# Optimization experiments

Measured on AMD Instinct MI355X. Metric: run time of the kernel, lower is better.

Reference implementation:

```python
import jax, jax.numpy as jnp
import numpy as np

B, N, H = 32, 1024, 256
ALPHA = 0.2  # leaky relu slope
NEG_INF = -1e12


def setup_inputs() -> dict:
    key = jax.random.key(0)
    k1, k2, k3, k4, k5, k6 = jax.random.split(key, 6)
    inp = jax.random.normal(k1, (B, N, H), dtype=jnp.float32)
    A = (jax.random.uniform(k2, (B, N, N)) < 0.05).astype(jnp.float32)
    l = jnp.sort(jax.random.randint(k3, (B, 2), 0, N), axis=1)
    # xavier-uniform(gain=1.414) approximated; exact init values are irrelevant for correctness
    lim_w = 1.414 * np.sqrt(6.0 / (H + H))
    W_i = jax.random.uniform(k4, (H, H), minval=-lim_w, maxval=lim_w, dtype=jnp.float32)
    W_c = jax.random.uniform(k5, (H, H), minval=-lim_w, maxval=lim_w, dtype=jnp.float32)
    lim_a = 1.414 * np.sqrt(6.0 / (2 * H + 1))
    a = jax.random.uniform(k6, (2 * H, 1), minval=-lim_a, maxval=lim_a, dtype=jnp.float32)
    return {"inp": inp, "A": A, "l": l, "W_i": W_i, "W_c": W_c, "a": a}


def reference(inp, A, l, W_i, W_c, a):
    # eval mode: dropout is identity (training=False)
    n = inp.shape[1]
    h = inp.shape[2]
    Wh_i = jnp.einsum('bnh,he->bne', inp, W_i)
    Wh_c = jnp.einsum('bnh,he->bne', inp, W_c)
    # vectorized replacement of the per-batch Wh[index][i:j] = Wh_i[index][i:j] loop
    idx = jnp.arange(n)
    sel = (idx[None, :] >= l[:, 0:1]) & (idx[None, :] < l[:, 1:2])  # [B,N]
    Wh = jnp.where(sel[:, :, None], Wh_i, Wh_c)
    # additive attention scores
    Wh1 = Wh @ a[:h, :]  # [B,N,1]
    Wh2 = Wh @ a[h:, :]  # [B,N,1]
    A_ = A + jnp.eye(n, dtype=A.dtype)
    e = jax.nn.leaky_relu((Wh1 + jnp.swapaxes(Wh2, 1, 2)) * A_, ALPHA)
    att = jnp.where(A_ > 0, e, NEG_INF)
    att = jax.nn.softmax(att, axis=2)
    h_prime = jnp.einsum('bnm,bme->bne', att, Wh)
    return jax.nn.elu(h_prime)  # concat=True
```

## Files before the change

kernel.cpp:

```cpp
#include <hip/hip_runtime.h>
#include <hip/hip_bf16.h>
#include <stdint.h>

#define B_ 32
#define N_ 1024
#define H_ 256

typedef short bf16x8 __attribute__((ext_vector_type(8)));
typedef float floatx4 __attribute__((ext_vector_type(4)));

__device__ inline unsigned short f2bs(float x) {
    __hip_bfloat16 h = __float2bfloat16(x);
    return __builtin_bit_cast(unsigned short, h);
}

__global__ __launch_bounds__(256)
void k_uvec(const float* __restrict__ Wi, const float* __restrict__ Wc,
            const float* __restrict__ a, float* __restrict__ U) {
    int k = blockIdx.x;
    int t = threadIdx.x;
    float wi = Wi[k * H_ + t];
    float wc = Wc[k * H_ + t];
    float a1 = a[t], a2 = a[H_ + t];
    float p0 = wi * a1, p1 = wc * a1, p2 = wi * a2, p3 = wc * a2;
    for (int off = 32; off; off >>= 1) {
        p0 += __shfl_xor(p0, off);
        p1 += __shfl_xor(p1, off);
        p2 += __shfl_xor(p2, off);
        p3 += __shfl_xor(p3, off);
    }
    __shared__ float red[4][4];
    int w = t >> 6;
    if ((t & 63) == 0) { red[w][0] = p0; red[w][1] = p1; red[w][2] = p2; red[w][3] = p3; }
    __syncthreads();
    if (t == 0) {
        U[0 * H_ + k] = red[0][0] + red[1][0] + red[2][0] + red[3][0];
        U[1 * H_ + k] = red[0][1] + red[1][1] + red[2][1] + red[3][1];
        U[2 * H_ + k] = red[0][2] + red[1][2] + red[2][2] + red[3][2];
        U[3 * H_ + k] = red[0][3] + red[1][3] + red[2][3] + red[3][3];
    }
}

__global__ __launch_bounds__(256)
void k_prep(const float* __restrict__ Wi, const float* __restrict__ Wc,
            unsigned short* __restrict__ WtFi, unsigned short* __restrict__ WtFc) {
    __shared__ float tile[64][65];
    int mat = blockIdx.x >> 4;
    int tr = ((blockIdx.x >> 2) & 3) * 64;
    int tc = (blockIdx.x & 3) * 64;
    const float* W = mat ? Wc : Wi;
    unsigned short* WtF = mat ? WtFc : WtFi;
    int t = threadIdx.x;
    int rr = t >> 2, c4 = (t & 3) * 16;
    const float* src = W + (size_t)(tr + rr) * H_ + tc + c4;
#pragma unroll
    for (int j = 0; j < 4; ++j) {
        float4 v = *reinterpret_cast<const float4*>(src + j * 4);
        tile[rr][c4 + 4 * j + 0] = v.x;
        tile[rr][c4 + 4 * j + 1] = v.y;
        tile[rr][c4 + 4 * j + 2] = v.z;
        tile[rr][c4 + 4 * j + 3] = v.w;
    }
    __syncthreads();
#pragma unroll
    for (int h = 0; h < 2; ++h) {
        int s = h * 256 + t;
        int ksl = s >> 8;
        int cl  = (s >> 6) & 3;
        int ll  = s & 63;
        int m16v = ll & 15, quadv = ll >> 4;
        int nloc = cl * 16 + m16v;
        int kb = ksl * 32 + quadv * 8;
        unsigned int pk[4];
#pragma unroll
        for (int jj = 0; jj < 4; ++jj) {
            unsigned short lo = f2bs(tile[kb + 2 * jj][nloc]);
            unsigned short hi = f2bs(tile[kb + 2 * jj + 1][nloc]);
            pk[jj] = (unsigned int)lo | ((unsigned int)hi << 16);
        }
        int ksg = (tr >> 5) + ksl;
        int cg  = (tc >> 4) + cl;
        *reinterpret_cast<uint4*>(WtF + ((size_t)(ksg * 16 + cg) * 64 + ll) * 8) =
            *reinterpret_cast<uint4*>(pk);
    }
}

__global__ __launch_bounds__(256)
void k_gemm(const float* __restrict__ inp, const int* __restrict__ l,
            const unsigned short* __restrict__ WtFi, const unsigned short* __restrict__ WtFc,
            unsigned short* __restrict__ WhF, const float* __restrict__ U,
            float* __restrict__ Wh1, float* __restrict__ Wh2) {
    __shared__ unsigned short bbuf[2][4096];
    int blk = blockIdx.x;
    int b  = blk >> 5;
    int r0 = ((blk >> 1) & 15) * 64;
    int n0 = (blk & 1) * 128;
    int t = threadIdx.x;
    int w = t >> 6;
    int lane = t & 63;
    int quad = lane >> 4, m16 = lane & 15;
    int rowb = r0 + w * 16;

    int l0 = l[2 * b], l1 = l[2 * b + 1];
    bool allI = (l0 <= r0) && (r0 + 64 <= l1);
    bool allC = (l1 <= r0) || (l0 >= r0 + 64);
    int npass = (allI || allC) ? 1 : 2;

    int row = rowb + m16;
    bool sel = (row >= l0) && (row < l1);
    const float* xrow = inp + ((size_t)(b * N_ + row)) * H_;
    const float* u1 = U + (sel ? 0 : H_);
    const float* u2 = U + 2 * H_ + (sel ? 0 : H_);
    bool doWh = (n0 == 0);
    float d1 = 0.f, d2 = 0.f;

    unsigned short* fb = WhF + (size_t)b * (N_ * H_);
    int cb = n0 >> 4;

    int j0 = rowb + quad * 4;
    int ksO = j0 >> 5;
    int laneF = m16 + 16 * ((j0 & 31) >> 3);
    int jj0 = j0 & 7;

    for (int pass = 0; pass < npass; ++pass) {
        const unsigned short* WtF =
            (npass == 1) ? (allI ? WtFi : WtFc) : (pass == 0 ? WtFi : WtFc);
        const unsigned short* gbase = WtF + cb * 512;

        floatx4 acc[8];
#pragma unroll
        for (int c = 0; c < 8; ++c) acc[c] = (floatx4){0.f, 0.f, 0.f, 0.f};

        {
            uint4 v0 = *reinterpret_cast<const uint4*>(gbase + (size_t)t * 8);
            uint4 v1 = *reinterpret_cast<const uint4*>(gbase + (size_t)(256 + t) * 8);
            *reinterpret_cast<uint4*>(&bbuf[0][t * 8]) = v0;
            *reinterpret_cast<uint4*>(&bbuf[0][(256 + t) * 8]) = v1;
        }
        for (int ks = 0; ks < 8; ++ks) {
            __syncthreads();
            uint4 v0, v1;
            if (ks < 7) {
                v0 = *reinterpret_cast<const uint4*>(gbase + (size_t)(ks + 1) * 8192 + t * 8);
                v1 = *reinterpret_cast<const uint4*>(gbase + (size_t)(ks + 1) * 8192 + (256 + t) * 8);
            }
            const float4 xa = *reinterpret_cast<const float4*>(xrow + ks * 32 + quad * 8);
            const float4 xb = *reinterpret_cast<const float4*>(xrow + ks * 32 + quad * 8 + 4);
            if (pass == 0 && doWh) {
                const float4 ua = *reinterpret_cast<const float4*>(u1 + ks * 32 + quad * 8);
                const float4 ub = *reinterpret_cast<const float4*>(u1 + ks * 32 + quad * 8 + 4);
                const float4 va = *reinterpret_cast<const float4*>(u2 + ks * 32 + quad * 8);
                const float4 vb = *reinterpret_cast<const float4*>(u2 + ks * 32 + quad * 8 + 4);
                d1 += xa.x * ua.x + xa.y * ua.y + xa.z * ua.z + xa.w * ua.w
                    + xb.x * ub.x + xb.y * ub.y + xb.z * ub.z + xb.w * ub.w;
                d2 += xa.x * va.x + xa.y * va.y + xa.z * va.z + xa.w * va.w
                    + xb.x * vb.x + xb.y * vb.y + xb.z * vb.z + xb.w * vb.w;
            }
            unsigned int pk0 = (unsigned int)f2bs(xa.x) | ((unsigned int)f2bs(xa.y) << 16);
            unsigned int pk1 = (unsigned int)f2bs(xa.z) | ((unsigned int)f2bs(xa.w) << 16);
            unsigned int pk2 = (unsigned int)f2bs(xb.x) | ((unsigned int)f2bs(xb.y) << 16);
            unsigned int pk3 = (unsigned int)f2bs(xb.z) | ((unsigned int)f2bs(xb.w) << 16);
            uint4 apk = {pk0, pk1, pk2, pk3};
            bf16x8 af = __builtin_bit_cast(bf16x8, apk);

            const unsigned short* bptr = &bbuf[ks & 1][lane * 8];
#pragma unroll
            for (int c = 0; c < 8; ++c) {
                bf16x8 bfr = *reinterpret_cast<const bf16x8*>(bptr + c * 512);
                acc[c] = __builtin_amdgcn_mfma_f32_16x16x32_bf16(af, bfr, acc[c], 0, 0, 0);
            }
            if (ks < 7) {
                *reinterpret_cast<uint4*>(&bbuf[(ks + 1) & 1][t * 8]) = v0;
                *reinterpret_cast<uint4*>(&bbuf[(ks + 1) & 1][(256 + t) * 8]) = v1;
            }
        }
        __syncthreads();

#pragma unroll
        for (int c = 0; c < 8; ++c) {
            size_t base = ((size_t)((ksO * 16 + cb + c) * 64) + laneF) * 8 + jj0;
            if (npass == 1) {
                unsigned int lo = (unsigned int)f2bs(acc[c][0]) | ((unsigned int)f2bs(acc[c][1]) << 16);
                unsigned int hi = (unsigned int)f2bs(acc[c][2]) | ((unsigned int)f2bs(acc[c][3]) << 16);
                uint2 v = {lo, hi};
                *reinterpret_cast<uint2*>(fb + base) = v;
            } else {
                bool want[4]; bool all = true, none = true;
#pragma unroll
                for (int r = 0; r < 4; ++r) {
                    int j = j0 + r;
                    bool s2 = (j >= l0) && (j < l1);
                    want[r] = (pass == 0) ? s2 : !s2;
                    all = all && want[r]; none = none && !want[r];
                }
                if (all) {
                    unsigned int lo = (unsigned int)f2bs(acc[c][0]) | ((unsigned int)f2bs(acc[c][1]) << 16);
                    unsigned int hi = (unsigned int)f2bs(acc[c][2]) | ((unsigned int)f2bs(acc[c][3]) << 16);
                    uint2 v = {lo, hi};
                    *reinterpret_cast<uint2*>(fb + base) = v;
                } else if (!none) {
#pragma unroll
                    for (int r = 0; r < 4; ++r)
                        if (want[r]) fb[base + r] = f2bs(acc[c][r]);
                }
            }
        }
    }

    if (doWh) {
        d1 += __shfl_xor(d1, 16); d1 += __shfl_xor(d1, 32);
        d2 += __shfl_xor(d2, 16); d2 += __shfl_xor(d2, 32);
        if (quad == 0) {
            Wh1[b * N_ + rowb + m16] = d1;
            Wh2[b * N_ + rowb + m16] = d2;
        }
    }
}

__global__ __launch_bounds__(256)
void k_attn(const float* __restrict__ A, const float* __restrict__ Wh1,
            const float* __restrict__ Wh2, const unsigned short* __restrict__ WhF,
            float* __restrict__ out) {
    __shared__ unsigned short pfrag[2][32 * 520];
    __shared__ float scl[32];
    int t = threadIdx.x, w = t >> 6, lane = t & 63;
    int bi = blockIdx.x;
    int b = (bi & 7) * 4 + (bi >> 8);
    int tile = (bi >> 3) & 31;
    int rowbase = tile * 32;

    const float* Wh2b = Wh2 + b * N_;
    float4 w2v[4];
#pragma unroll
    for (int ch = 0; ch < 4; ++ch)
        w2v[ch] = *reinterpret_cast<const float4*>(Wh2b + ch * 256 + lane * 4);

    int ksl = lane >> 3;
    int q2 = (lane >> 1) & 3;
    int jj0 = (lane & 1) * 4;

#pragma unroll
    for (int tt = 0; tt < 2; ++tt) {
#pragma unroll
        for (int q = 0; q < 4; ++q) {
            int m = w * 4 + q;
            int i = rowbase + tt * 16 + m;
            float wh1 = Wh1[b * N_ + i];
            const float* Arow = A + ((size_t)(b * N_ + i)) * N_;
            float e[16];
            float lmax = -1e30f;
#pragma unroll
            for (int ch = 0; ch < 4; ++ch) {
                float4 av = *reinterpret_cast<const float4*>(Arow + ch * 256 + lane * 4);
                if ((i >> 2) == (ch * 64 + lane)) ((float*)&av)[i & 3] += 1.0f;
                float aa[4] = {av.x, av.y, av.z, av.w};
                float ww[4] = {w2v[ch].x, w2v[ch].y, w2v[ch].z, w2v[ch].w};
#pragma unroll
                for (int c = 0; c < 4; ++c) {
                    float p = (wh1 + ww[c]) * aa[c];
                    float lv = fmaxf(p, 0.2f * p);
                    e[ch * 4 + c] = aa[c] > 0.f ? lv : -1e30f;
                    lmax = fmaxf(lmax, e[ch * 4 + c]);
                }
            }
            for (int off = 32; off; off >>= 1) lmax = fmaxf(lmax, __shfl_xor(lmax, off));

            float lsum = 0.f;
            unsigned int pk[8];
#pragma unroll
            for (int h2 = 0; h2 < 8; ++h2) {
                float p0 = e[2 * h2]     > -1e29f ? __expf(e[2 * h2]     - lmax) : 0.f;
                float p1 = e[2 * h2 + 1] > -1e29f ? __expf(e[2 * h2 + 1] - lmax) : 0.f;
                lsum += p0 + p1;
                pk[h2] = (unsigned int)f2bs(p0) | ((unsigned int)f2bs(p1) << 16);
            }
            for (int off = 32; off; off >>= 1) lsum += __shfl_xor(lsum, off);
            if (lane == 0) scl[tt * 16 + m] = 1.0f / lsum;

#pragma unroll
            for (int ch = 0; ch < 4; ++ch) {
                int ks = ch * 8 + ksl;
                uint2 v = {pk[2 * ch], pk[2 * ch + 1]};
                *reinterpret_cast<uint2*>(pfrag[tt] + ks * 520 + (m + 16 * q2) * 8 + jj0) = v;
            }
        }
    }
    __syncthreads();

    const unsigned short* WB = WhF + (size_t)b * (N_ * H_);
    floatx4 acc0[4], acc1[4];
#pragma unroll
    for (int cc = 0; cc < 4; ++cc) {
        acc0[cc] = (floatx4){0.f, 0.f, 0.f, 0.f};
        acc1[cc] = (floatx4){0.f, 0.f, 0.f, 0.f};
    }
#pragma unroll 2
    for (int ks = 0; ks < 32; ++ks) {
        bf16x8 af0 = *reinterpret_cast<const bf16x8*>(pfrag[0] + ks * 520 + lane * 8);
        bf16x8 af1 = *reinterpret_cast<const bf16x8*>(pfrag[1] + ks * 520 + lane * 8);
#pragma unroll
        for (int cc = 0; cc < 4; ++cc) {
            int c = w * 4 + cc;
            bf16x8 bfv = *reinterpret_cast<const bf16x8*>(
                WB + ((size_t)((ks * 16 + c) * 64 + lane)) * 8);
            acc0[cc] = __builtin_amdgcn_mfma_f32_16x16x32_bf16(af0, bfv, acc0[cc], 0, 0, 0);
            acc1[cc] = __builtin_amdgcn_mfma_f32_16x16x32_bf16(af1, bfv, acc1[cc], 0, 0, 0);
        }
    }

    int quad = lane >> 4, m16 = lane & 15;
#pragma unroll
    for (int cc = 0; cc < 4; ++cc) {
        int col = (w * 4 + cc) * 16 + m16;
#pragma unroll
        for (int r = 0; r < 4; ++r) {
            int m = quad * 4 + r;
            float v0 = acc0[cc][r] * scl[m];
            v0 = v0 > 0.f ? v0 : __expf(v0) - 1.0f;
            out[((size_t)(b * N_ + rowbase + m)) * H_ + col] = v0;
            float v1 = acc1[cc][r] * scl[16 + m];
            v1 = v1 > 0.f ? v1 : __expf(v1) - 1.0f;
            out[((size_t)(b * N_ + rowbase + 16 + m)) * H_ + col] = v1;
        }
    }
}

extern "C" void kernel_launch(void* const* d_in, const int* in_sizes, int n_in,
                              void* d_out, int out_size, void* d_ws, size_t ws_size,
                              hipStream_t stream) {
    const float* inp = (const float*)d_in[0];
    const float* A   = (const float*)d_in[1];
    const int*   l   = (const int*)d_in[2];
    const float* Wi  = (const float*)d_in[3];
    const float* Wc  = (const float*)d_in[4];
    const float* a   = (const float*)d_in[5];
    float* out = (float*)d_out;

    char* ws = (char*)d_ws;
    size_t off = 0;
    unsigned short* WhF  = (unsigned short*)(ws + off); off += (size_t)B_ * N_ * H_ * 2;
    float* Wh1 = (float*)(ws + off); off += (size_t)B_ * N_ * 4;
    float* Wh2 = (float*)(ws + off); off += (size_t)B_ * N_ * 4;
    float* U   = (float*)(ws + off); off += 4 * H_ * 4;
    unsigned short* WtFi = (unsigned short*)(ws + off); off += (size_t)H_ * H_ * 2;
    unsigned short* WtFc = (unsigned short*)(ws + off); off += (size_t)H_ * H_ * 2;

    k_uvec<<<H_, 256, 0, stream>>>(Wi, Wc, a, U);
    k_prep<<<32, 256, 0, stream>>>(Wi, Wc, WtFi, WtFc);
    k_gemm<<<B_ * 16 * 2, 256, 0, stream>>>(inp, l, WtFi, WtFc, WhF, U, Wh1, Wh2);
    k_attn<<<B_ * (N_ / 32), 256, 0, stream>>>(A, Wh1, Wh2, WhF, out);
}
```

Measured before the change: 289.1 us.

## Drop softmax max/sum reductions; compute row sums via MFMA with ones and swizzle LDS

The softmax no longer subtracts a row maximum. It exponentiates the leaky-relu scores directly, which removes the two cross-lane shuffle reductions and the register array of scores per row. Row sums are now computed inside the MFMA loop by multiplying the probability fragments with a vector of bf16 ones, so no LDS scale array is needed. The LDS layout of the probability fragments is XOR-swizzled to reduce bank conflicts. Skipping the max subtraction risks overflow for large scores, and the sums are now taken from bf16-rounded values.

```diff
diff --git a/kernel.cpp b/kernel.cpp
--- a/kernel.cpp
+++ b/kernel.cpp
@@ -5,6 +5,7 @@
 #define B_ 32
 #define N_ 1024
 #define H_ 256
+#define PF_PITCH 520
 
 typedef short bf16x8 __attribute__((ext_vector_type(8)));
 typedef float floatx4 __attribute__((ext_vector_type(4)));
@@ -221,8 +222,7 @@
 void k_attn(const float* __restrict__ A, const float* __restrict__ Wh1,
             const float* __restrict__ Wh2, const unsigned short* __restrict__ WhF,
             float* __restrict__ out) {
-    __shared__ unsigned short pfrag[2][32 * 520];
-    __shared__ float scl[32];
+    __shared__ unsigned short pfrag[2][32 * PF_PITCH];
     int t = threadIdx.x, w = t >> 6, lane = t & 63;
     int bi = blockIdx.x;
     int b = (bi & 7) * 4 + (bi >> 8);
@@ -247,48 +247,40 @@
             int i = rowbase + tt * 16 + m;
             float wh1 = Wh1[b * N_ + i];
             const float* Arow = A + ((size_t)(b * N_ + i)) * N_;
-            float e[16];
-            float lmax = -1e30f;
+            int s = m + 16 * q2;
+            int sw = s ^ ((s >> 3) & 7);
+            int sls = sw * 8 + jj0;
 #pragma unroll
             for (int ch = 0; ch < 4; ++ch) {
                 float4 av = *reinterpret_cast<const float4*>(Arow + ch * 256 + lane * 4);
                 if ((i >> 2) == (ch * 64 + lane)) ((float*)&av)[i & 3] += 1.0f;
                 float aa[4] = {av.x, av.y, av.z, av.w};
                 float ww[4] = {w2v[ch].x, w2v[ch].y, w2v[ch].z, w2v[ch].w};
+                float p[4];
 #pragma unroll
                 for (int c = 0; c < 4; ++c) {
-                    float p = (wh1 + ww[c]) * aa[c];
-                    float lv = fmaxf(p, 0.2f * p);
-                    e[ch * 4 + c] = aa[c] > 0.f ? lv : -1e30f;
-                    lmax = fmaxf(lmax, e[ch * 4 + c]);
+                    float e  = (wh1 + ww[c]) * aa[c];
+                    float lv = fmaxf(e, 0.2f * e);
+                    p[c] = aa[c] > 0.f ? __expf(lv) : 0.f;
                 }
-            }
-            for (int off = 32; off; off >>= 1) lmax = fmaxf(lmax, __shfl_xor(lmax, off));
-
-            float lsum = 0.f;
-            unsigned int pk[8];
-#pragma unroll
-            for (int h2 = 0; h2 < 8; ++h2) {
-                float p0 = e[2 * h2]     > -1e29f ? __expf(e[2 * h2]     - lmax) : 0.f;
-                float p1 = e[2 * h2 + 1] > -1e29f ? __expf(e[2 * h2 + 1] - lmax) : 0.f;
-                lsum += p0 + p1;
-                pk[h2] = (unsigned int)f2bs(p0) | ((unsigned int)f2bs(p1) << 16);
-            }
-            for (int off = 32; off; off >>= 1) lsum += __shfl_xor(lsum, off);
-            if (lane == 0) scl[tt * 16 + m] = 1.0f / lsum;
-
-#pragma unroll
-            for (int ch = 0; ch < 4; ++ch) {
+                unsigned int lo = (unsigned int)f2bs(p[0]) | ((unsigned int)f2bs(p[1]) << 16);
+                unsigned int hi = (unsigned int)f2bs(p[2]) | ((unsigned int)f2bs(p[3]) << 16);
+                uint2 v = {lo, hi};
                 int ks = ch * 8 + ksl;
-                uint2 v = {pk[2 * ch], pk[2 * ch + 1]};
-                *reinterpret_cast<uint2*>(pfrag[tt] + ks * 520 + (m + 16 * q2) * 8 + jj0) = v;
+                *reinterpret_cast<uint2*>(pfrag[tt] + ks * PF_PITCH + sls) = v;
             }
         }
     }
     __syncthreads();
 
     const unsigned short* WB = WhF + (size_t)b * (N_ * H_);
-    floatx4 acc0[4], acc1[4];
+    int rs = (lane ^ ((lane >> 3) & 7)) * 8;
+    unsigned short oneb = f2bs(1.0f);
+    bf16x8 bones = {(short)oneb, (short)oneb, (short)oneb, (short)oneb,
+                    (short)oneb, (short)oneb, (short)oneb, (short)oneb};
+    floatx4 acc0[4], acc1[4], sum0, sum1;
+    sum0 = (floatx4){0.f, 0.f, 0.f, 0.f};
+    sum1 = (floatx4){0.f, 0.f, 0.f, 0.f};
 #pragma unroll
     for (int cc = 0; cc < 4; ++cc) {
         acc0[cc] = (floatx4){0.f, 0.f, 0.f, 0.f};
@@ -296,8 +288,10 @@
     }
 #pragma unroll 2
     for (int ks = 0; ks < 32; ++ks) {
-        bf16x8 af0 = *reinterpret_cast<const bf16x8*>(pfrag[0] + ks * 520 + lane * 8);
-        bf16x8 af1 = *reinterpret_cast<const bf16x8*>(pfrag[1] + ks * 520 + lane * 8);
+        bf16x8 af0 = *reinterpret_cast<const bf16x8*>(pfrag[0] + ks * PF_PITCH + rs);
+        bf16x8 af1 = *reinterpret_cast<const bf16x8*>(pfrag[1] + ks * PF_PITCH + rs);
+        sum0 = __builtin_amdgcn_mfma_f32_16x16x32_bf16(af0, bones, sum0, 0, 0, 0);
+        sum1 = __builtin_amdgcn_mfma_f32_16x16x32_bf16(af1, bones, sum1, 0, 0, 0);
 #pragma unroll
         for (int cc = 0; cc < 4; ++cc) {
             int c = w * 4 + cc;
@@ -309,16 +303,22 @@
     }
 
     int quad = lane >> 4, m16 = lane & 15;
+    float inv0[4], inv1[4];
+#pragma unroll
+    for (int r = 0; r < 4; ++r) {
+        inv0[r] = 1.0f / sum0[r];
+        inv1[r] = 1.0f / sum1[r];
+    }
 #pragma unroll
     for (int cc = 0; cc < 4; ++cc) {
         int col = (w * 4 + cc) * 16 + m16;
 #pragma unroll
         for (int r = 0; r < 4; ++r) {
             int m = quad * 4 + r;
-            float v0 = acc0[cc][r] * scl[m];
+            float v0 = acc0[cc][r] * inv0[r];
             v0 = v0 > 0.f ? v0 : __expf(v0) - 1.0f;
             out[((size_t)(b * N_ + rowbase + m)) * H_ + col] = v0;
-            float v1 = acc1[cc][r] * scl[16 + m];
+            float v1 = acc1[cc][r] * inv1[r];
             v1 = v1 > 0.f ? v1 : __expf(v1) - 1.0f;
             out[((size_t)(b * N_ + rowbase + 16 + m)) * H_ + col] = v1;
         }
```

Result: faster. 280.9 us (-2.8%).
